# Kernel optimization log

Measured on AMD Instinct MI355X. Metric: run time of the kernel, lower is better.

Reference implementation:

```python
import jax, jax.numpy as jnp
import numpy as np

K = 5       # strip kernel size
DIL = 1     # dilation
G = 4       # groups


def _strip_att(x, conv_w, inside_all, lamb_l, lamb_h, horizontal):
    # x: (n, c, h, w); conv_w: (G*K, c); inside_all: (c,1,1); lamb_*: (c,)
    n, c, h, w = x.shape
    # global avg pool -> 1x1 conv -> tanh filter, shaped (n, G, 1, K, 1, 1)
    f = jnp.tanh(jnp.einsum('nc,oc->no', x.mean(axis=(2, 3)), conv_w))
    f = f.reshape(n, G, 1, K, 1, 1)
    pad = DIL * (K - 1) // 2
    if horizontal:
        xp = jnp.pad(x, ((0, 0), (0, 0), (0, 0), (pad, pad)), mode='reflect')
        # K shifted strips along W (equivalent to F.unfold with kernel (1,K))
        wins = jnp.stack([xp[:, :, :, i * DIL:i * DIL + w] for i in range(K)], axis=2)
        gapx = x.mean(axis=3, keepdims=True)   # (n,c,h,1)
    else:
        xp = jnp.pad(x, ((0, 0), (0, 0), (pad, pad), (0, 0)), mode='reflect')
        wins = jnp.stack([xp[:, :, i * DIL:i * DIL + h, :] for i in range(K)], axis=2)
        gapx = x.mean(axis=2, keepdims=True)   # (n,c,1,w)
    # (n,c,K,h,w) -> (n,G,c//G,K,h,w); weighted sum over kernel positions
    wins = wins.reshape(n, G, c // G, K, h, w)
    out = (wins * f).sum(axis=3).reshape(n, c, h, w)
    out_low = (out * (inside_all + 1.0) - inside_all * gapx) * lamb_l[:, None, None]
    out_high = x * (lamb_h[:, None, None] + 1.0)
    return out_low + out_high


def setup_inputs() -> dict:
    key = jax.random.key(0)
    ks = jax.random.split(key, 11)
    C = 128
    x = jax.random.normal(ks[0], (4, C, 256, 256), dtype=jnp.float32)
    s = 0.1
    return {
        'x': x,
        'conv_h': jax.random.normal(ks[1], (G * K, C), dtype=jnp.float32) * s,
        'inside_h': jax.random.normal(ks[2], (C, 1, 1), dtype=jnp.float32) * s,
        'lamb_l_h': jax.random.normal(ks[3], (C,), dtype=jnp.float32) * s,
        'lamb_h_h': jax.random.normal(ks[4], (C,), dtype=jnp.float32) * s,
        'conv_v': jax.random.normal(ks[5], (G * K, C), dtype=jnp.float32) * s,
        'inside_v': jax.random.normal(ks[6], (C, 1, 1), dtype=jnp.float32) * s,
        'lamb_l_v': jax.random.normal(ks[7], (C,), dtype=jnp.float32) * s,
        'lamb_h_v': jax.random.normal(ks[8], (C,), dtype=jnp.float32) * s,
        'gamma': jax.random.normal(ks[9], (C, 1, 1), dtype=jnp.float32) * s,
        'beta': 1.0 + jax.random.normal(ks[10], (C, 1, 1), dtype=jnp.float32) * s,
    }


def reference(x, conv_h, inside_h, lamb_l_h, lamb_h_h,
              conv_v, inside_v, lamb_l_v, lamb_h_v, gamma, beta):
    out = _strip_att(x, conv_h, inside_h, lamb_l_h, lamb_h_h, horizontal=True)
    out = _strip_att(out, conv_v, inside_v, lamb_l_v, lamb_h_v, horizontal=False)
    return gamma * out + x * beta
```

## Files before the change

kernel.cpp:

```cpp
#include <hip/hip_runtime.h>
#include <math.h>

#define NB   4
#define CC   128
#define HH   256
#define WW   256
#define HWSZ (HH * WW)
#define NC   (NB * CC)
#define GK   20

__device__ __forceinline__ float wave_reduce_sum(float v) {
#pragma unroll
    for (int o = 1; o < 64; o <<= 1) v += __shfl_xor(v, o, 64);
    return v;
}

__global__ __launch_bounds__(256) void k_reduce(const float4* __restrict__ x4,
                                                float* __restrict__ rowsum,
                                                float* __restrict__ colsum_part,
                                                float* __restrict__ planesum_part) {
    const int bx = blockIdx.x;
    const int b = bx >> 2;
    const int chunk = bx & 3;
    const int t = threadIdx.x;
    const int wv = t >> 6;
    const int l = t & 63;
    const float4* plane = x4 + (size_t)b * (HWSZ / 4);
    const int r0 = chunk * 64 + wv * 16;

    float4 cs = make_float4(0.f, 0.f, 0.f, 0.f);
#pragma unroll 4
    for (int i = 0; i < 16; ++i) {
        float4 v = plane[(r0 + i) * (WW / 4) + l];
        cs.x += v.x; cs.y += v.y; cs.z += v.z; cs.w += v.w;
        float rs = wave_reduce_sum((v.x + v.y) + (v.z + v.w));
        if (l == 0) rowsum[b * HH + r0 + i] = rs;
    }

    __shared__ float colpart[4][WW];
    colpart[wv][4 * l + 0] = cs.x;
    colpart[wv][4 * l + 1] = cs.y;
    colpart[wv][4 * l + 2] = cs.z;
    colpart[wv][4 * l + 3] = cs.w;
    __syncthreads();
    float c = (colpart[0][t] + colpart[1][t]) + (colpart[2][t] + colpart[3][t]);
    colsum_part[(size_t)b * 4 * WW + chunk * WW + t] = c;

    float p = wave_reduce_sum(c);
    __shared__ float pr[4];
    if (l == 0) pr[wv] = p;
    __syncthreads();
    if (t == 0) planesum_part[b * 4 + chunk] = (pr[0] + pr[1]) + (pr[2] + pr[3]);
}

__global__ __launch_bounds__(256) void k_small(const float* __restrict__ colsum_part,
                                               const float* __restrict__ planesum_part,
                                               const float* __restrict__ conv_h,
                                               const float* __restrict__ inside_h,
                                               const float* __restrict__ lamb_l_h,
                                               const float* __restrict__ lamb_h_h,
                                               const float* __restrict__ conv_v,
                                               float* __restrict__ planesum,
                                               float* __restrict__ f_h_out,
                                               float* __restrict__ f_v_out) {
    __shared__ float meanx[NC];
    __shared__ float psum[NC];
    __shared__ float fh[NB * GK];
    __shared__ float mo1[NC];
    const int t = threadIdx.x;

    for (int i = t; i < NC; i += 256) {
        float S = (planesum_part[i * 4 + 0] + planesum_part[i * 4 + 1]) +
                  (planesum_part[i * 4 + 2] + planesum_part[i * 4 + 3]);
        psum[i] = S;
        planesum[i] = S;
        meanx[i] = S * (1.f / HWSZ);
    }
    __syncthreads();

    if (t < NB * GK) {
        const int n = t / GK, o = t % GK;
        float acc = 0.f;
        for (int c = 0; c < CC; ++c) acc += meanx[n * CC + c] * conv_h[o * CC + c];
        float v = tanhf(acc);
        fh[t] = v;
        f_h_out[t] = v;
    }
    __syncthreads();

    for (int i = t; i < NC; i += 256) {
        const int n = i >> 7, c = i & (CC - 1), g = c >> 5;
        const float* f = &fh[n * GK + g * 5];
        const float S = psum[i];
        const float* col = colsum_part + (size_t)i * 4 * WW;
        auto csum = [&](int w) {
            return (col[0 * WW + w] + col[1 * WW + w]) +
                   (col[2 * WW + w] + col[3 * WW + w]);
        };
        const float c0 = csum(0), c1 = csum(1), c2 = csum(2);
        const float c253 = csum(253), c254 = csum(254), c255 = csum(255);
        const float s0 = S + c1 + c2 - c254 - c255;
        const float s1 = S + c1 - c255;
        const float s2 = S;
        const float s3 = S + c254 - c0;
        const float s4 = S + c253 + c254 - c0 - c1;
        const float convmean =
            (f[0] * s0 + f[1] * s1 + f[2] * s2 + f[3] * s3 + f[4] * s4) * (1.f / HWSZ);
        const float A = (inside_h[c] + 1.f) * lamb_l_h[c];
        const float B = inside_h[c] * lamb_l_h[c];
        const float Cq = lamb_h_h[c] + 1.f;
        mo1[i] = A * convmean + (Cq - B) * meanx[i];
    }
    __syncthreads();

    if (t < NB * GK) {
        const int n = t / GK, o = t % GK;
        float acc = 0.f;
        for (int c = 0; c < CC; ++c) acc += mo1[n * CC + c] * conv_v[o * CC + c];
        f_v_out[t] = tanhf(acc);
    }
}

#define TH 64

__global__ __launch_bounds__(256) void k_main(const float* __restrict__ x,
                                              const float* __restrict__ rowsum,
                                              const float* __restrict__ colsum_part,
                                              const float* __restrict__ planesum,
                                              const float* __restrict__ f_h,
                                              const float* __restrict__ f_v,
                                              const float* __restrict__ inside_h,
                                              const float* __restrict__ lamb_l_h,
                                              const float* __restrict__ lamb_h_h,
                                              const float* __restrict__ inside_v,
                                              const float* __restrict__ lamb_l_v,
                                              const float* __restrict__ lamb_h_v,
                                              const float* __restrict__ gamma,
                                              const float* __restrict__ beta,
                                              float* __restrict__ out) {
    const int b = blockIdx.x >> 2;
    const int tile = blockIdx.x & 3;
    const int h0 = tile * TH;
    const int n = b >> 7, c = b & (CC - 1), g = c >> 5;
    const int t = threadIdx.x;
    const int wv = t >> 6;
    const int l = t & 63;

    float fh[5], fv[5];
#pragma unroll
    for (int k = 0; k < 5; ++k) {
        fh[k] = f_h[n * GK + g * 5 + k];
        fv[k] = f_v[n * GK + g * 5 + k];
    }
    const float Ah = (inside_h[c] + 1.f) * lamb_l_h[c];
    const float Bh = inside_h[c] * lamb_l_h[c];
    const float Ch = lamb_h_h[c] + 1.f;
    const float Av = (inside_v[c] + 1.f) * lamb_l_v[c];
    const float Bv = inside_v[c] * lamb_l_v[c];
    const float Cv = lamb_h_v[c] + 1.f;
    const float gm = gamma[c], bt = beta[c];
    const float meanx = planesum[b] * (1.f / HWSZ);

    __shared__ float lcol[WW + 4];
    {
        const float* col = colsum_part + (size_t)b * 4 * WW;
        float cm = ((col[0 * WW + t] + col[1 * WW + t]) +
                    (col[2 * WW + t] + col[3 * WW + t])) * (1.f / HH);
        lcol[t + 2] = cm;
        if (t < 2) {
            int w = 2 - t;
            lcol[t] = ((col[0 * WW + w] + col[1 * WW + w]) +
                       (col[2 * WW + w] + col[3 * WW + w])) * (1.f / HH);
        }
        if (t >= WW - 2) {
            int w = 2 * WW - 4 - t;
            lcol[t + 4] = ((col[0 * WW + w] + col[1 * WW + w]) +
                           (col[2 * WW + w] + col[3 * WW + w])) * (1.f / HH);
        }
    }
    __syncthreads();
    float gx[4];
    {
        float q[8];
#pragma unroll
        for (int d = 0; d < 8; ++d) q[d] = lcol[4 * l + d];
#pragma unroll
        for (int d = 0; d < 4; ++d) {
            gx[d] = Ah * (fh[0] * q[d] + fh[1] * q[d + 1] + fh[2] * q[d + 2] +
                          fh[3] * q[d + 3] + fh[4] * q[d + 4]) -
                    Bh * meanx + Ch * q[d + 2];
        }
    }

    __shared__ float hring[16][WW];
    const float* plane = x + (size_t)b * HWSZ;
    float* oplane = out + (size_t)b * HWSZ;

    auto hrOf = [&](int j) -> int {
        int hs = h0 - 4 + 4 * j + wv;
        return hs < 0 ? -hs : (hs > HH - 1 ? 2 * HH - 2 - hs : hs);
    };

    int hrn = hrOf(0);
    float4 vnext = *(const float4*)&plane[hrn * WW + 4 * l];
    float ghnext = rowsum[b * HH + hrn];
    float4 xprev = make_float4(0.f, 0.f, 0.f, 0.f);

    for (int j = 0; j <= 17; ++j) {
        float4 v;
        if (j <= 16) {
            v = vnext;
            const float gh = ghnext * (1.f / WW);
            if (j < 16) {
                hrn = hrOf(j + 1);
                vnext = *(const float4*)&plane[hrn * WW + 4 * l];
                ghnext = rowsum[b * HH + hrn];
            }

            float xm2 = __shfl_up(v.z, 1);
            float xm1 = __shfl_up(v.w, 1);
            float xp4 = __shfl_down(v.x, 1);
            float xp5 = __shfl_down(v.y, 1);
            if (l == 0)  { xm2 = v.z; xm1 = v.y; }
            if (l == 63) { xp4 = v.z; xp5 = v.y; }

            const float h0v = fh[0] * xm2 + fh[1] * xm1 + fh[2] * v.x + fh[3] * v.y + fh[4] * v.z;
            const float h1v = fh[0] * xm1 + fh[1] * v.x + fh[2] * v.y + fh[3] * v.z + fh[4] * v.w;
            const float h2v = fh[0] * v.x + fh[1] * v.y + fh[2] * v.z + fh[3] * v.w + fh[4] * xp4;
            const float h3v = fh[0] * v.y + fh[1] * v.z + fh[2] * v.w + fh[3] * xp4 + fh[4] * xp5;

            float4 r1;
            r1.x = Ah * h0v - Bh * gh + Ch * v.x;
            r1.y = Ah * h1v - Bh * gh + Ch * v.y;
            r1.z = Ah * h2v - Bh * gh + Ch * v.z;
            r1.w = Ah * h3v - Bh * gh + Ch * v.w;

            const int hs = h0 - 4 + 4 * j + wv;
            *(float4*)&hring[hs & 15][4 * l] = r1;
        }
        __syncthreads();

        if (j >= 2) {
            const int O = h0 - 8 + 4 * j + wv;
            float ax = 0.f, ay = 0.f, az = 0.f, aw = 0.f;
            float4 rc;
#pragma unroll
            for (int k = 0; k < 5; ++k) {
                int vrow = O + k - 2;
                int vr = vrow < 0 ? -vrow : (vrow > HH - 1 ? 2 * HH - 2 - vrow : vrow);
                float4 hv = *(const float4*)&hring[vr & 15][4 * l];
                ax += fv[k] * hv.x;
                ay += fv[k] * hv.y;
                az += fv[k] * hv.z;
                aw += fv[k] * hv.w;
                if (k == 2) rc = hv;
            }
            float4 res;
            res.x = gm * (Av * ax - Bv * gx[0] + Cv * rc.x) + bt * xprev.x;
            res.y = gm * (Av * ay - Bv * gx[1] + Cv * rc.y) + bt * xprev.y;
            res.z = gm * (Av * az - Bv * gx[2] + Cv * rc.z) + bt * xprev.z;
            res.w = gm * (Av * aw - Bv * gx[3] + Cv * rc.w) + bt * xprev.w;
            *(float4*)&oplane[O * WW + 4 * l] = res;
        }

        if (j <= 16) xprev = v;
    }
}

extern "C" void kernel_launch(void* const* d_in, const int* in_sizes, int n_in,
                              void* d_out, int out_size, void* d_ws, size_t ws_size,
                              hipStream_t stream) {
    const float* x        = (const float*)d_in[0];
    const float* conv_h   = (const float*)d_in[1];
    const float* inside_h = (const float*)d_in[2];
    const float* lamb_l_h = (const float*)d_in[3];
    const float* lamb_h_h = (const float*)d_in[4];
    const float* conv_v   = (const float*)d_in[5];
    const float* inside_v = (const float*)d_in[6];
    const float* lamb_l_v = (const float*)d_in[7];
    const float* lamb_h_v = (const float*)d_in[8];
    const float* gamma    = (const float*)d_in[9];
    const float* beta     = (const float*)d_in[10];
    float* out = (float*)d_out;

    float* ws = (float*)d_ws;
    float* rowsum        = ws;
    float* colsum_part   = ws + 131072;
    float* planesum_part = ws + 655360;
    float* planesum      = ws + 657408;
    float* f_h           = ws + 657920;
    float* f_v           = ws + 658000;

    k_reduce<<<NC * 4, 256, 0, stream>>>((const float4*)x, rowsum, colsum_part,
                                         planesum_part);
    k_small<<<1, 256, 0, stream>>>(colsum_part, planesum_part, conv_h, inside_h,
                                   lamb_l_h, lamb_h_h, conv_v, planesum, f_h, f_v);
    k_main<<<NC * 4, 256, 0, stream>>>(x, rowsum, colsum_part, planesum, f_h, f_v,
                                       inside_h, lamb_l_h, lamb_h_h,
                                       inside_v, lamb_l_v, lamb_h_v,
                                       gamma, beta, out);
}
```

Before: 85.51 us.

## Fold single-block filter kernel into main kernel and recompute row sums in-loop

Removes the single-block k_small launch by having every k_main block recompute the per-batch tanh filters (both horizontal and vertical) from the partial plane and column sums in shared memory. Row sums are no longer written by k_reduce; k_main instead computes each row's mean with a wave reduction on the row it already loaded. This removes a serialized one-block kernel and its launch gap, plus the rowsum global traffic. In exchange, each of the 2048 main blocks repeats a small matrix-vector product and extra column-sum reads, and gains a wave reduction per row.

```diff
diff --git a/kernel.cpp b/kernel.cpp
--- a/kernel.cpp
+++ b/kernel.cpp
@@ -16,7 +16,6 @@
 }
 
 __global__ __launch_bounds__(256) void k_reduce(const float4* __restrict__ x4,
-                                                float* __restrict__ rowsum,
                                                 float* __restrict__ colsum_part,
                                                 float* __restrict__ planesum_part) {
     const int bx = blockIdx.x;
@@ -33,8 +32,6 @@
     for (int i = 0; i < 16; ++i) {
         float4 v = plane[(r0 + i) * (WW / 4) + l];
         cs.x += v.x; cs.y += v.y; cs.z += v.z; cs.w += v.w;
-        float rs = wave_reduce_sum((v.x + v.y) + (v.z + v.w));
-        if (l == 0) rowsum[b * HH + r0 + i] = rs;
     }
 
     __shared__ float colpart[4][WW];
@@ -53,82 +50,13 @@
     if (t == 0) planesum_part[b * 4 + chunk] = (pr[0] + pr[1]) + (pr[2] + pr[3]);
 }
 
-__global__ __launch_bounds__(256) void k_small(const float* __restrict__ colsum_part,
-                                               const float* __restrict__ planesum_part,
-                                               const float* __restrict__ conv_h,
-                                               const float* __restrict__ inside_h,
-                                               const float* __restrict__ lamb_l_h,
-                                               const float* __restrict__ lamb_h_h,
-                                               const float* __restrict__ conv_v,
-                                               float* __restrict__ planesum,
-                                               float* __restrict__ f_h_out,
-                                               float* __restrict__ f_v_out) {
-    __shared__ float meanx[NC];
-    __shared__ float psum[NC];
-    __shared__ float fh[NB * GK];
-    __shared__ float mo1[NC];
-    const int t = threadIdx.x;
-
-    for (int i = t; i < NC; i += 256) {
-        float S = (planesum_part[i * 4 + 0] + planesum_part[i * 4 + 1]) +
-                  (planesum_part[i * 4 + 2] + planesum_part[i * 4 + 3]);
-        psum[i] = S;
-        planesum[i] = S;
-        meanx[i] = S * (1.f / HWSZ);
-    }
-    __syncthreads();
-
-    if (t < NB * GK) {
-        const int n = t / GK, o = t % GK;
-        float acc = 0.f;
-        for (int c = 0; c < CC; ++c) acc += meanx[n * CC + c] * conv_h[o * CC + c];
-        float v = tanhf(acc);
-        fh[t] = v;
-        f_h_out[t] = v;
-    }
-    __syncthreads();
-
-    for (int i = t; i < NC; i += 256) {
-        const int n = i >> 7, c = i & (CC - 1), g = c >> 5;
-        const float* f = &fh[n * GK + g * 5];
-        const float S = psum[i];
-        const float* col = colsum_part + (size_t)i * 4 * WW;
-        auto csum = [&](int w) {
-            return (col[0 * WW + w] + col[1 * WW + w]) +
-                   (col[2 * WW + w] + col[3 * WW + w]);
-        };
-        const float c0 = csum(0), c1 = csum(1), c2 = csum(2);
-        const float c253 = csum(253), c254 = csum(254), c255 = csum(255);
-        const float s0 = S + c1 + c2 - c254 - c255;
-        const float s1 = S + c1 - c255;
-        const float s2 = S;
-        const float s3 = S + c254 - c0;
-        const float s4 = S + c253 + c254 - c0 - c1;
-        const float convmean =
-            (f[0] * s0 + f[1] * s1 + f[2] * s2 + f[3] * s3 + f[4] * s4) * (1.f / HWSZ);
-        const float A = (inside_h[c] + 1.f) * lamb_l_h[c];
-        const float B = inside_h[c] * lamb_l_h[c];
-        const float Cq = lamb_h_h[c] + 1.f;
-        mo1[i] = A * convmean + (Cq - B) * meanx[i];
-    }
-    __syncthreads();
-
-    if (t < NB * GK) {
-        const int n = t / GK, o = t % GK;
-        float acc = 0.f;
-        for (int c = 0; c < CC; ++c) acc += mo1[n * CC + c] * conv_v[o * CC + c];
-        f_v_out[t] = tanhf(acc);
-    }
-}
-
 #define TH 64
 
 __global__ __launch_bounds__(256) void k_main(const float* __restrict__ x,
-                                              const float* __restrict__ rowsum,
                                               const float* __restrict__ colsum_part,
-                                              const float* __restrict__ planesum,
-                                              const float* __restrict__ f_h,
-                                              const float* __restrict__ f_v,
+                                              const float* __restrict__ planesum_part,
+                                              const float* __restrict__ conv_h,
+                                              const float* __restrict__ conv_v,
                                               const float* __restrict__ inside_h,
                                               const float* __restrict__ lamb_l_h,
                                               const float* __restrict__ lamb_h_h,
@@ -146,11 +74,86 @@
     const int wv = t >> 6;
     const int l = t & 63;
 
+    __shared__ float meanx_s[CC];
+    __shared__ float psum_s[CC];
+    __shared__ float fh_all[GK];
+    __shared__ float mo1_s[CC];
+    __shared__ float fv_s[5];
+
+    const float* pp = planesum_part + n * CC * 4;
+    if (t < CC) {
+        float S = (pp[t * 4 + 0] + pp[t * 4 + 1]) + (pp[t * 4 + 2] + pp[t * 4 + 3]);
+        psum_s[t] = S;
+        meanx_s[t] = S * (1.f / HWSZ);
+    }
+    __syncthreads();
+
+    if (t < GK) {
+        const float4* w4 = (const float4*)(conv_h + t * CC);
+        float acc = 0.f;
+#pragma unroll 8
+        for (int i = 0; i < CC / 4; ++i) {
+            float4 w = w4[i];
+            acc += w.x * meanx_s[4 * i] + w.y * meanx_s[4 * i + 1] +
+                   w.z * meanx_s[4 * i + 2] + w.w * meanx_s[4 * i + 3];
+        }
+        fh_all[t] = tanhf(acc);
+    }
+    __syncthreads();
+
+    if (t < CC) {
+        const float* f = &fh_all[(t >> 5) * 5];
+        const float S = psum_s[t];
+        const float* col = colsum_part + (size_t)(n * CC + t) * 4 * WW;
+        auto csum = [&](int w) {
+            return (col[0 * WW + w] + col[1 * WW + w]) +
+                   (col[2 * WW + w] + col[3 * WW + w]);
+        };
+        const float c0 = csum(0), c1 = csum(1), c2 = csum(2);
+        const float c253 = csum(253), c254 = csum(254), c255 = csum(255);
+        const float s0 = S + c1 + c2 - c254 - c255;
+        const float s1 = S + c1 - c255;
+        const float s3 = S + c254 - c0;
+        const float s4 = S + c253 + c254 - c0 - c1;
+        const float convmean =
+            (f[0] * s0 + f[1] * s1 + f[2] * S + f[3] * s3 + f[4] * s4) * (1.f / HWSZ);
+        const float A = (inside_h[t] + 1.f) * lamb_l_h[t];
+        const float B = inside_h[t] * lamb_l_h[t];
+        const float Cq = lamb_h_h[t] + 1.f;
+        mo1_s[t] = A * convmean + (Cq - B) * meanx_s[t];
+    }
+    __syncthreads();
+
+    if (t < 5) {
+        const float4* w4 = (const float4*)(conv_v + (g * 5 + t) * CC);
+        float acc = 0.f;
+#pragma unroll 8
+        for (int i = 0; i < CC / 4; ++i) {
+            float4 w = w4[i];
+            acc += w.x * mo1_s[4 * i] + w.y * mo1_s[4 * i + 1] +
+                   w.z * mo1_s[4 * i + 2] + w.w * mo1_s[4 * i + 3];
+        }
+        fv_s[t] = tanhf(acc);
+    }
+
+    __shared__ float lcol[WW + 4];
+    {
+        const float* col = colsum_part + (size_t)b * 4 * WW;
+        auto csum = [&](int w) {
+            return ((col[0 * WW + w] + col[1 * WW + w]) +
+                    (col[2 * WW + w] + col[3 * WW + w])) * (1.f / HH);
+        };
+        lcol[t + 2] = csum(t);
+        if (t < 2) lcol[t] = csum(2 - t);
+        if (t >= WW - 2) lcol[t + 4] = csum(2 * WW - 4 - t);
+    }
+    __syncthreads();
+
     float fh[5], fv[5];
 #pragma unroll
     for (int k = 0; k < 5; ++k) {
-        fh[k] = f_h[n * GK + g * 5 + k];
-        fv[k] = f_v[n * GK + g * 5 + k];
+        fh[k] = fh_all[g * 5 + k];
+        fv[k] = fv_s[k];
     }
     const float Ah = (inside_h[c] + 1.f) * lamb_l_h[c];
     const float Bh = inside_h[c] * lamb_l_h[c];
@@ -159,26 +162,8 @@
     const float Bv = inside_v[c] * lamb_l_v[c];
     const float Cv = lamb_h_v[c] + 1.f;
     const float gm = gamma[c], bt = beta[c];
-    const float meanx = planesum[b] * (1.f / HWSZ);
-
-    __shared__ float lcol[WW + 4];
-    {
-        const float* col = colsum_part + (size_t)b * 4 * WW;
-        float cm = ((col[0 * WW + t] + col[1 * WW + t]) +
-                    (col[2 * WW + t] + col[3 * WW + t])) * (1.f / HH);
-        lcol[t + 2] = cm;
-        if (t < 2) {
-            int w = 2 - t;
-            lcol[t] = ((col[0 * WW + w] + col[1 * WW + w]) +
-                       (col[2 * WW + w] + col[3 * WW + w])) * (1.f / HH);
-        }
-        if (t >= WW - 2) {
-            int w = 2 * WW - 4 - t;
-            lcol[t + 4] = ((col[0 * WW + w] + col[1 * WW + w]) +
-                           (col[2 * WW + w] + col[3 * WW + w])) * (1.f / HH);
-        }
-    }
-    __syncthreads();
+    const float meanx = meanx_s[c];
+
     float gx[4];
     {
         float q[8];
@@ -196,26 +181,24 @@
     const float* plane = x + (size_t)b * HWSZ;
     float* oplane = out + (size_t)b * HWSZ;
 
-    auto hrOf = [&](int j) -> int {
+    auto rowptr = [&](int j) -> const float4* {
         int hs = h0 - 4 + 4 * j + wv;
-        return hs < 0 ? -hs : (hs > HH - 1 ? 2 * HH - 2 - hs : hs);
+        int hr = hs < 0 ? -hs : (hs > HH - 1 ? 2 * HH - 2 - hs : hs);
+        return (const float4*)&plane[hr * WW + 4 * l];
     };
 
-    int hrn = hrOf(0);
-    float4 vnext = *(const float4*)&plane[hrn * WW + 4 * l];
-    float ghnext = rowsum[b * HH + hrn];
+    float4 vnext = *rowptr(0);
     float4 xprev = make_float4(0.f, 0.f, 0.f, 0.f);
 
     for (int j = 0; j <= 17; ++j) {
         float4 v;
         if (j <= 16) {
             v = vnext;
-            const float gh = ghnext * (1.f / WW);
-            if (j < 16) {
-                hrn = hrOf(j + 1);
-                vnext = *(const float4*)&plane[hrn * WW + 4 * l];
-                ghnext = rowsum[b * HH + hrn];
-            }
+            if (j < 16) vnext = *rowptr(j + 1);
+
+            float rsum = (v.x + v.y) + (v.z + v.w);
+            rsum = wave_reduce_sum(rsum);
+            const float gh = rsum * (1.f / WW);
 
             float xm2 = __shfl_up(v.z, 1);
             float xm1 = __shfl_up(v.w, 1);
@@ -284,18 +267,13 @@
     float* out = (float*)d_out;
 
     float* ws = (float*)d_ws;
-    float* rowsum        = ws;
-    float* colsum_part   = ws + 131072;
-    float* planesum_part = ws + 655360;
-    float* planesum      = ws + 657408;
-    float* f_h           = ws + 657920;
-    float* f_v           = ws + 658000;
-
-    k_reduce<<<NC * 4, 256, 0, stream>>>((const float4*)x, rowsum, colsum_part,
+    float* colsum_part   = ws;
+    float* planesum_part = ws + 524288;
+
+    k_reduce<<<NC * 4, 256, 0, stream>>>((const float4*)x, colsum_part,
                                          planesum_part);
-    k_small<<<1, 256, 0, stream>>>(colsum_part, planesum_part, conv_h, inside_h,
-                                   lamb_l_h, lamb_h_h, conv_v, planesum, f_h, f_v);
-    k_main<<<NC * 4, 256, 0, stream>>>(x, rowsum, colsum_part, planesum, f_h, f_v,
+    k_main<<<NC * 4, 256, 0, stream>>>(x, colsum_part, planesum_part,
+                                       conv_h, conv_v,
                                        inside_h, lamb_l_h, lamb_h_h,
                                        inside_v, lamb_l_v, lamb_h_v,
                                        gamma, beta, out);
```

New measurement: 82.94 us. 3.0% less time.

## Fold small filter kernel into reduce via last-block counter, recompute row sums inline

Applied to the files above, without the earlier changes.

Removes the separate single-block k_small launch. The last k_reduce block to finish, detected with an atomic counter and threadfences, now computes the tanh filters. The row-sum buffer is also dropped: k_main computes each row mean with a wave reduction on the row it has already loaded, instead of writing and re-reading a rowsum array. This saves one launch and some global traffic. In exchange it adds a memset launch, atomic and fence overhead in every reduce block, and a serial tail where one block does the filter work.

```diff
diff --git a/kernel.cpp b/kernel.cpp
--- a/kernel.cpp
+++ b/kernel.cpp
@@ -8,6 +8,7 @@
 #define HWSZ (HH * WW)
 #define NC   (NB * CC)
 #define GK   20
+#define NBLK (NC * 4)
 
 __device__ __forceinline__ float wave_reduce_sum(float v) {
 #pragma unroll
@@ -16,9 +17,17 @@
 }
 
 __global__ __launch_bounds__(256) void k_reduce(const float4* __restrict__ x4,
-                                                float* __restrict__ rowsum,
                                                 float* __restrict__ colsum_part,
-                                                float* __restrict__ planesum_part) {
+                                                float* __restrict__ planesum_part,
+                                                float* __restrict__ planesum,
+                                                const float* __restrict__ conv_h,
+                                                const float* __restrict__ inside_h,
+                                                const float* __restrict__ lamb_l_h,
+                                                const float* __restrict__ lamb_h_h,
+                                                const float* __restrict__ conv_v,
+                                                float* __restrict__ f_h_out,
+                                                float* __restrict__ f_v_out,
+                                                unsigned int* __restrict__ counter) {
     const int bx = blockIdx.x;
     const int b = bx >> 2;
     const int chunk = bx & 3;
@@ -33,8 +42,6 @@
     for (int i = 0; i < 16; ++i) {
         float4 v = plane[(r0 + i) * (WW / 4) + l];
         cs.x += v.x; cs.y += v.y; cs.z += v.z; cs.w += v.w;
-        float rs = wave_reduce_sum((v.x + v.y) + (v.z + v.w));
-        if (l == 0) rowsum[b * HH + r0 + i] = rs;
     }
 
     __shared__ float colpart[4][WW];
@@ -50,29 +57,24 @@
     __shared__ float pr[4];
     if (l == 0) pr[wv] = p;
     __syncthreads();
-    if (t == 0) planesum_part[b * 4 + chunk] = (pr[0] + pr[1]) + (pr[2] + pr[3]);
-}
-
-__global__ __launch_bounds__(256) void k_small(const float* __restrict__ colsum_part,
-                                               const float* __restrict__ planesum_part,
-                                               const float* __restrict__ conv_h,
-                                               const float* __restrict__ inside_h,
-                                               const float* __restrict__ lamb_l_h,
-                                               const float* __restrict__ lamb_h_h,
-                                               const float* __restrict__ conv_v,
-                                               float* __restrict__ planesum,
-                                               float* __restrict__ f_h_out,
-                                               float* __restrict__ f_v_out) {
+    if (t == 0) pr[0] = (pr[0] + pr[1]) + (pr[2] + pr[3]);
+    __syncthreads();
+    if (t == 0) planesum_part[bx] = pr[0];
+
+    __shared__ unsigned int is_last;
+    __threadfence();
+    if (t == 0) is_last = (atomicAdd(counter, 1u) == NBLK - 1);
+    __syncthreads();
+    if (!is_last) return;
+    __threadfence();
+
     __shared__ float meanx[NC];
-    __shared__ float psum[NC];
     __shared__ float fh[NB * GK];
     __shared__ float mo1[NC];
-    const int t = threadIdx.x;
 
     for (int i = t; i < NC; i += 256) {
         float S = (planesum_part[i * 4 + 0] + planesum_part[i * 4 + 1]) +
                   (planesum_part[i * 4 + 2] + planesum_part[i * 4 + 3]);
-        psum[i] = S;
         planesum[i] = S;
         meanx[i] = S * (1.f / HWSZ);
     }
@@ -81,7 +83,7 @@
     if (t < NB * GK) {
         const int n = t / GK, o = t % GK;
         float acc = 0.f;
-        for (int c = 0; c < CC; ++c) acc += meanx[n * CC + c] * conv_h[o * CC + c];
+        for (int cc = 0; cc < CC; ++cc) acc += meanx[n * CC + cc] * conv_h[o * CC + cc];
         float v = tanhf(acc);
         fh[t] = v;
         f_h_out[t] = v;
@@ -89,9 +91,9 @@
     __syncthreads();
 
     for (int i = t; i < NC; i += 256) {
-        const int n = i >> 7, c = i & (CC - 1), g = c >> 5;
+        const int n = i >> 7, cc = i & (CC - 1), g = cc >> 5;
         const float* f = &fh[n * GK + g * 5];
-        const float S = psum[i];
+        const float S = planesum[i];
         const float* col = colsum_part + (size_t)i * 4 * WW;
         auto csum = [&](int w) {
             return (col[0 * WW + w] + col[1 * WW + w]) +
@@ -101,14 +103,13 @@
         const float c253 = csum(253), c254 = csum(254), c255 = csum(255);
         const float s0 = S + c1 + c2 - c254 - c255;
         const float s1 = S + c1 - c255;
-        const float s2 = S;
         const float s3 = S + c254 - c0;
         const float s4 = S + c253 + c254 - c0 - c1;
         const float convmean =
-            (f[0] * s0 + f[1] * s1 + f[2] * s2 + f[3] * s3 + f[4] * s4) * (1.f / HWSZ);
-        const float A = (inside_h[c] + 1.f) * lamb_l_h[c];
-        const float B = inside_h[c] * lamb_l_h[c];
-        const float Cq = lamb_h_h[c] + 1.f;
+            (f[0] * s0 + f[1] * s1 + f[2] * S + f[3] * s3 + f[4] * s4) * (1.f / HWSZ);
+        const float A = (inside_h[cc] + 1.f) * lamb_l_h[cc];
+        const float B = inside_h[cc] * lamb_l_h[cc];
+        const float Cq = lamb_h_h[cc] + 1.f;
         mo1[i] = A * convmean + (Cq - B) * meanx[i];
     }
     __syncthreads();
@@ -116,7 +117,7 @@
     if (t < NB * GK) {
         const int n = t / GK, o = t % GK;
         float acc = 0.f;
-        for (int c = 0; c < CC; ++c) acc += mo1[n * CC + c] * conv_v[o * CC + c];
+        for (int cc = 0; cc < CC; ++cc) acc += mo1[n * CC + cc] * conv_v[o * CC + cc];
         f_v_out[t] = tanhf(acc);
     }
 }
@@ -124,7 +125,6 @@
 #define TH 64
 
 __global__ __launch_bounds__(256) void k_main(const float* __restrict__ x,
-                                              const float* __restrict__ rowsum,
                                               const float* __restrict__ colsum_part,
                                               const float* __restrict__ planesum,
                                               const float* __restrict__ f_h,
@@ -164,19 +164,13 @@
     __shared__ float lcol[WW + 4];
     {
         const float* col = colsum_part + (size_t)b * 4 * WW;
-        float cm = ((col[0 * WW + t] + col[1 * WW + t]) +
-                    (col[2 * WW + t] + col[3 * WW + t])) * (1.f / HH);
-        lcol[t + 2] = cm;
-        if (t < 2) {
-            int w = 2 - t;
-            lcol[t] = ((col[0 * WW + w] + col[1 * WW + w]) +
-                       (col[2 * WW + w] + col[3 * WW + w])) * (1.f / HH);
-        }
-        if (t >= WW - 2) {
-            int w = 2 * WW - 4 - t;
-            lcol[t + 4] = ((col[0 * WW + w] + col[1 * WW + w]) +
-                           (col[2 * WW + w] + col[3 * WW + w])) * (1.f / HH);
-        }
+        auto csum = [&](int w) {
+            return ((col[0 * WW + w] + col[1 * WW + w]) +
+                    (col[2 * WW + w] + col[3 * WW + w])) * (1.f / HH);
+        };
+        lcol[t + 2] = csum(t);
+        if (t < 2) lcol[t] = csum(2 - t);
+        if (t >= WW - 2) lcol[t + 4] = csum(2 * WW - 4 - t);
     }
     __syncthreads();
     float gx[4];
@@ -196,26 +190,24 @@
     const float* plane = x + (size_t)b * HWSZ;
     float* oplane = out + (size_t)b * HWSZ;
 
-    auto hrOf = [&](int j) -> int {
+    auto rowptr = [&](int j) -> const float4* {
         int hs = h0 - 4 + 4 * j + wv;
-        return hs < 0 ? -hs : (hs > HH - 1 ? 2 * HH - 2 - hs : hs);
+        int hr = hs < 0 ? -hs : (hs > HH - 1 ? 2 * HH - 2 - hs : hs);
+        return (const float4*)&plane[hr * WW + 4 * l];
     };
 
-    int hrn = hrOf(0);
-    float4 vnext = *(const float4*)&plane[hrn * WW + 4 * l];
-    float ghnext = rowsum[b * HH + hrn];
+    float4 vnext = *rowptr(0);
     float4 xprev = make_float4(0.f, 0.f, 0.f, 0.f);
 
     for (int j = 0; j <= 17; ++j) {
         float4 v;
         if (j <= 16) {
             v = vnext;
-            const float gh = ghnext * (1.f / WW);
-            if (j < 16) {
-                hrn = hrOf(j + 1);
-                vnext = *(const float4*)&plane[hrn * WW + 4 * l];
-                ghnext = rowsum[b * HH + hrn];
-            }
+            if (j < 16) vnext = *rowptr(j + 1);
+
+            float rsum = (v.x + v.y) + (v.z + v.w);
+            rsum = wave_reduce_sum(rsum);
+            const float gh = rsum * (1.f / WW);
 
             float xm2 = __shfl_up(v.z, 1);
             float xm1 = __shfl_up(v.w, 1);
@@ -284,18 +276,19 @@
     float* out = (float*)d_out;
 
     float* ws = (float*)d_ws;
-    float* rowsum        = ws;
-    float* colsum_part   = ws + 131072;
-    float* planesum_part = ws + 655360;
-    float* planesum      = ws + 657408;
-    float* f_h           = ws + 657920;
-    float* f_v           = ws + 658000;
-
-    k_reduce<<<NC * 4, 256, 0, stream>>>((const float4*)x, rowsum, colsum_part,
-                                         planesum_part);
-    k_small<<<1, 256, 0, stream>>>(colsum_part, planesum_part, conv_h, inside_h,
-                                   lamb_l_h, lamb_h_h, conv_v, planesum, f_h, f_v);
-    k_main<<<NC * 4, 256, 0, stream>>>(x, rowsum, colsum_part, planesum, f_h, f_v,
+    float* colsum_part   = ws;
+    float* planesum_part = ws + 524288;
+    float* planesum      = ws + 526336;
+    float* f_h           = ws + 526848;
+    float* f_v           = ws + 526928;
+    unsigned int* counter = (unsigned int*)(ws + 527008);
+
+    hipMemsetAsync(counter, 0, sizeof(unsigned int), stream);
+    k_reduce<<<NBLK, 256, 0, stream>>>((const float4*)x, colsum_part,
+                                       planesum_part, planesum,
+                                       conv_h, inside_h, lamb_l_h, lamb_h_h,
+                                       conv_v, f_h, f_v, counter);
+    k_main<<<NC * 4, 256, 0, stream>>>(x, colsum_part, planesum, f_h, f_v,
                                        inside_h, lamb_l_h, lamb_h_h,
                                        inside_v, lamb_l_v, lamb_h_v,
                                        gamma, beta, out);
```

Result: slower. 336.0 us (+292.9%).
